# Performance work log

Hardware: AMD Instinct MI355X
Metric: run time of the kernel (lower is better)

Reference implementation:

```python
import jax, jax.numpy as jnp
import numpy as np

B, H, S, D = 2, 16, 2048, 128
BS = 128  # block_size
NB = S // BS  # num_blocks
SPARSITY_PROB = 0.5


def setup_inputs() -> dict:
    key = jax.random.key(0)
    kq, kk, kv, km = jax.random.split(key, 4)
    query = jax.random.normal(kq, (B, H, S, D), dtype=jnp.float32)
    k_ = jax.random.normal(kk, (B, H, S, D), dtype=jnp.float32)
    v_ = jax.random.normal(kv, (B, H, S, D), dtype=jnp.float32)
    # block pattern: rand < sparsity_prob, diagonal forced True (causal=False)
    block_mask = jax.random.uniform(km, (NB, NB)) < SPARSITY_PROB
    block_mask = block_mask | jnp.eye(NB, dtype=bool)
    return {"query": query, "key": k_, "value": v_,
            "block_mask": block_mask, "block_size": BS}


def reference(query, key, value, block_mask, block_size):
    b, h, s, d = query.shape
    nb = s // block_size
    scale = 1.0 / jnp.sqrt(jnp.float32(d))
    # reshape into blocks: (b, h, nb, bs, d)
    qb = query.reshape(b, h, nb, block_size, d)
    kb = key.reshape(b, h, nb, block_size, d)
    vb = value.reshape(b, h, nb, block_size, d)
    # per-(i,j)-block scores: (b, h, i, j, q, k)
    scores = jnp.einsum('bhiqd,bhjkd->bhijqk', qb, kb) * scale
    # IMPORTANT: softmax is taken independently within each block (axis=-1),
    # matching the original's per-block (non-merged) softmax.
    attn = jax.nn.softmax(scores, axis=-1)
    # zero out inactive blocks, then sum contributions over j
    attn = attn * block_mask[None, None, :, :, None, None].astype(attn.dtype)
    out = jnp.einsum('bhijqk,bhjkd->bhiqd', attn, vb)
    return out.reshape(b, h, s, d)
```

## Files before the change

kernel.cpp:

```cpp
#include <hip/hip_runtime.h>
#include <stdint.h>

#define CBDIM 256
#define WBDIM 256
#define DBDIM 512

#if __has_builtin(__builtin_amdgcn_permlane32_swap) && \
    __has_builtin(__builtin_amdgcn_permlane16_swap)
#define HAVE_PERMLANE_SWAP 1
#else
#define HAVE_PERMLANE_SWAP 0
#endif

typedef __attribute__((ext_vector_type(8))) short short8;
typedef __attribute__((ext_vector_type(4))) float f32x4;

__device__ __forceinline__ unsigned f2bf(float f) {
    union { float f; unsigned u; } a; a.f = f;
    unsigned r = a.u + 0x7fffu + ((a.u >> 16) & 1u);
    return (r >> 16) & 0xffffu;
}
__device__ __forceinline__ unsigned cvtpk_bf16(float a, float b) {
    unsigned r;
    asm("v_cvt_pk_bf16_f32 %0, %1, %2" : "=v"(r) : "v"(a), "v"(b));
    return r;
}
__device__ __forceinline__ float exp2_raw(float x) {
    float r;
    asm("v_exp_f32 %0, %1" : "=v"(r) : "v"(x));
    return r;
}
__device__ __forceinline__ float f4e(float4 v, int e) {
    return e == 0 ? v.x : e == 1 ? v.y : e == 2 ? v.z : v.w;
}
__device__ __forceinline__ unsigned u4e(uint4 v, int e) {
    return e == 0 ? v.x : e == 1 ? v.y : e == 2 ? v.z : v.w;
}
__device__ __forceinline__ uint2 shfl_u2(uint2 v, int src) {
    uint2 r;
    r.x = (unsigned)__shfl((int)v.x, src);
    r.y = (unsigned)__shfl((int)v.y, src);
    return r;
}
__device__ __forceinline__ float xor16_f(float x, int lane) {
#if HAVE_PERMLANE_SWAP
    unsigned u = __float_as_uint(x);
    auto r = __builtin_amdgcn_permlane16_swap(u, u, false, false);
    return __uint_as_float((lane & 16) ? r[0] : r[1]);
#else
    return __shfl_xor(x, 16);
#endif
}
__device__ __forceinline__ float xor32_f(float x, int lane) {
#if HAVE_PERMLANE_SWAP
    unsigned u = __float_as_uint(x);
    auto r = __builtin_amdgcn_permlane32_swap(u, u, false, false);
    return __uint_as_float((lane & 32) ? r[0] : r[1]);
#else
    return __shfl_xor(x, 32);
#endif
}
__device__ __forceinline__ bool detect_bf16(const void* p) {
    unsigned w = ((const unsigned*)p)[threadIdx.x & 63];
    unsigned lo = w & 0xffffu, ex = (lo >> 7) & 0xffu;
    bool pl = (lo == 0u) || (ex >= 0x68u && ex <= 0x86u);
    return __popcll(__ballot(pl)) >= 40;
}
__device__ __forceinline__ void gload_lds16(const void* g, void* l) {
    __builtin_amdgcn_global_load_lds(
        (const __attribute__((address_space(1))) void*)g,
        (__attribute__((address_space(3))) void*)l, 16, 0, 0);
}

__global__ __launch_bounds__(CBDIM)
void convert_fused(const void* __restrict__ Ksrc, const void* __restrict__ Vsrc,
                   uint4* __restrict__ Kw, uint4* __restrict__ Vt,
                   const unsigned char* __restrict__ Mb, int* __restrict__ order,
                   int nIdsK)
{
    const int tid = threadIdx.x;
    const int b = blockIdx.x;
    if (b < 512) {
        bool isBf = detect_bf16(Vsrc);
        if (b == 0 && tid < 64) {
            int tt = tid;
            unsigned mu = ((const unsigned*)Mb)[tt];
            bool maskByte = (__ballot((mu & 0xFFFFFF00u) != 0u) != 0ull);
            int cnt = 0;
            if (tt < 16)
                for (int j = 0; j < 16; ++j) {
                    bool a = maskByte ? (Mb[tt * 16 + j] != 0)
                                      : (((const int*)Mb)[tt * 16 + j] != 0);
                    cnt += a ? 1 : 0;
                }
            int rank = 0;
            for (int j = 0; j < 16; ++j) {
                int cj = __shfl(cnt, j);
                if (cj > cnt || (cj == cnt && j < tt)) ++rank;
            }
            if (tt < 16) order[rank] = tt;
        }
        const size_t kb = (size_t)b * 16384;
        char* base = (char*)(Vt + (size_t)b * 2048);
#pragma unroll
        for (int it = 0; it < 2; ++it) {
            int id = it * CBDIM + tid, pp = id & 31, dc = id >> 5;
            if (isBf) {
                const unsigned short* vb = (const unsigned short*)Vsrc + kb
                                           + (size_t)(4 * pp) * 128 + dc * 8;
                uint4 r0 = *(const uint4*)(vb);
                uint4 r1 = *(const uint4*)(vb + 128);
                uint4 r2 = *(const uint4*)(vb + 256);
                uint4 r3 = *(const uint4*)(vb + 384);
#pragma unroll
                for (int e = 0; e < 8; ++e) {
                    unsigned h0 = u4e(r0, e >> 1), h1 = u4e(r1, e >> 1);
                    unsigned h2 = u4e(r2, e >> 1), h3 = u4e(r3, e >> 1);
                    if (e & 1) { h0 >>= 16; h1 >>= 16; h2 >>= 16; h3 >>= 16; }
                    uint2 pk;
                    pk.x = (h0 & 0xffffu) | (h1 << 16);
                    pk.y = (h2 & 0xffffu) | (h3 << 16);
                    int d = dc * 8 + e;
                    *(uint2*)(base + d * 256 + (((pp >> 1) ^ (d & 7)) << 4)
                              + ((pp & 1) << 3)) = pk;
                }
            } else {
                const float* vb = (const float*)Vsrc + kb
                                  + (size_t)(4 * pp) * 128 + dc * 8;
                float4 ra[4], rb[4];
#pragma unroll
                for (int r = 0; r < 4; ++r) {
                    ra[r] = *(const float4*)(vb + (size_t)r * 128);
                    rb[r] = *(const float4*)(vb + (size_t)r * 128 + 4);
                }
#pragma unroll
                for (int e = 0; e < 8; ++e) {
                    float v0 = (e < 4) ? f4e(ra[0], e) : f4e(rb[0], e - 4);
                    float v1 = (e < 4) ? f4e(ra[1], e) : f4e(rb[1], e - 4);
                    float v2 = (e < 4) ? f4e(ra[2], e) : f4e(rb[2], e - 4);
                    float v3 = (e < 4) ? f4e(ra[3], e) : f4e(rb[3], e - 4);
                    uint2 pk;
                    pk.x = f2bf(v0) | (f2bf(v1) << 16);
                    pk.y = f2bf(v2) | (f2bf(v3) << 16);
                    int d = dc * 8 + e;
                    *(uint2*)(base + d * 256 + (((pp >> 1) ^ (d & 7)) << 4)
                              + ((pp & 1) << 3)) = pk;
                }
            }
        }
    } else {
        bool isBf = detect_bf16(Ksrc);
        int stride = ((int)gridDim.x - 512) * CBDIM;
        for (int id = (b - 512) * CBDIM + tid; id < nIdsK; id += stride) {
            int lid = id & 2047, tt = id >> 11;
            int r = lid >> 4, c = (lid & 15) ^ (r & 7);
            size_t eo = (size_t)tt * 16384 + (size_t)r * 128 + c * 8;
            uint4 w;
            if (isBf) {
                w = *(const uint4*)((const unsigned short*)Ksrc + eo);
            } else {
                const float* p = (const float*)Ksrc + eo;
                float4 f0 = *(const float4*)p, f1 = *(const float4*)(p + 4);
                w.x = f2bf(f0.x) | (f2bf(f0.y) << 16);
                w.y = f2bf(f0.z) | (f2bf(f0.w) << 16);
                w.z = f2bf(f1.x) | (f2bf(f1.y) << 16);
                w.w = f2bf(f1.z) | (f2bf(f1.w) << 16);
            }
            Kw[id] = w;
        }
    }
}

template<bool QF32>
__device__ __forceinline__ void attn_core(const void* Qv, const uint4* Kw,
                                          const uint4* Vt, unsigned actm,
                                          void* Ov, char* ldsK, char* ldsV,
                                          int bh, int i)
{
    constexpr int S = 2048, D = 128;
    const int tid  = threadIdx.x;
    const int lane = tid & 63;
    const int wv   = tid >> 6;
    const int quad = lane >> 4;
    const int l16  = lane & 15;

    const int qb0 = wv * 32;
    const size_t qrowbase = ((size_t)bh * S + (size_t)i * 128) * D;

    short8 qf[2][4];
#pragma unroll
    for (int nt = 0; nt < 2; ++nt) {
        int qrow = qb0 + nt * 16 + l16;
#pragma unroll
        for (int ks = 0; ks < 4; ++ks) {
            int dof = ks * 32 + quad * 8;
            if constexpr (QF32) {
                const float* qp = (const float*)Qv + qrowbase + (size_t)qrow * D + dof;
                float4 f0 = *(const float4*)qp;
                float4 f1 = *(const float4*)(qp + 4);
                short8 v;
                v[0] = (short)f2bf(f0.x); v[1] = (short)f2bf(f0.y);
                v[2] = (short)f2bf(f0.z); v[3] = (short)f2bf(f0.w);
                v[4] = (short)f2bf(f1.x); v[5] = (short)f2bf(f1.y);
                v[6] = (short)f2bf(f1.z); v[7] = (short)f2bf(f1.w);
                qf[nt][ks] = v;
            } else {
                qf[nt][ks] = *(const short8*)((const unsigned short*)Qv
                              + qrowbase + (size_t)qrow * D + dof);
            }
        }
    }

    f32x4 accO[2][8];
#pragma unroll
    for (int a = 0; a < 2; ++a)
#pragma unroll
        for (int b = 0; b < 8; ++b)
            accO[a][b] = (f32x4){0.f, 0.f, 0.f, 0.f};

    const float C2 = 0.08838834764831845f * 1.44269504088896f;

    auto STAGE = [&](const uint4* t, char* lds) {
#pragma unroll
        for (int it = 0; it < 8; ++it) {
            int id = it * WBDIM + tid;
            int lo = (it * WBDIM + wv * 64) * 16;
            gload_lds16(t + id, lds + lo);
        }
        asm volatile("" ::: "memory");
    };
    auto ktile = [&](int jj) { return Kw + (size_t)(bh * 16 + jj) * 2048; };
    auto vtile = [&](int jj) { return Vt + (size_t)(bh * 16 + jj) * 2048; };

    int j = (int)__builtin_ctz(actm);
    unsigned m = actm & (actm - 1);

    STAGE(ktile(j), ldsK);
    STAGE(vtile(j), ldsV);
    asm volatile("s_waitcnt vmcnt(8)" ::: "memory");
    asm volatile("s_barrier" ::: "memory");

    while (true) {
        int jn = m ? (int)__builtin_ctz(m) : -1;
        if (jn >= 0) m &= m - 1;

        f32x4 accS[2][8];
#pragma unroll
        for (int nt = 0; nt < 2; ++nt)
#pragma unroll
            for (int mt = 0; mt < 8; ++mt)
                accS[nt][mt] = (f32x4){0.f, 0.f, 0.f, 0.f};

#pragma unroll
        for (int mt = 0; mt < 8; ++mt) {
            int r = mt * 16 + l16;
            short8 kf[4];
#pragma unroll
            for (int ks = 0; ks < 4; ++ks) {
                int c = ks * 4 + quad;
                kf[ks] = *(const short8*)(ldsK + r * 256 + ((c ^ (r & 7)) << 4));
            }
            __builtin_amdgcn_s_setprio(1);
#pragma unroll
            for (int nt = 0; nt < 2; ++nt)
#pragma unroll
                for (int ks = 0; ks < 4; ++ks)
                    accS[nt][mt] = __builtin_amdgcn_mfma_f32_16x16x32_bf16(
                        kf[ks], qf[nt][ks], accS[nt][mt], 0, 0, 0);
            __builtin_amdgcn_s_setprio(0);
        }

        uint2 p2[2][8];
#pragma unroll
        for (int nt = 0; nt < 2; ++nt) {
            float ps[8];
#pragma unroll
            for (int mt = 0; mt < 8; ++mt) {
                f32x4 p;
#pragma unroll
                for (int rr = 0; rr < 4; ++rr)
                    p[rr] = exp2_raw(accS[nt][mt][rr] * C2);
                accS[nt][mt] = p;
                ps[mt] = (p[0] + p[1]) + (p[2] + p[3]);
            }
            float sum = ((ps[0] + ps[1]) + (ps[2] + ps[3]))
                      + ((ps[4] + ps[5]) + (ps[6] + ps[7]));
            sum += xor16_f(sum, lane);
            sum += xor32_f(sum, lane);
            float rinv = __builtin_amdgcn_rcpf(sum);
#pragma unroll
            for (int mt = 0; mt < 8; ++mt) {
                p2[nt][mt].x = cvtpk_bf16(accS[nt][mt][0] * rinv,
                                          accS[nt][mt][1] * rinv);
                p2[nt][mt].y = cvtpk_bf16(accS[nt][mt][2] * rinv,
                                          accS[nt][mt][3] * rinv);
            }
        }

        asm volatile("s_waitcnt vmcnt(0)" ::: "memory");
        asm volatile("s_barrier" ::: "memory");
        if (jn >= 0) STAGE(ktile(jn), ldsK);

#pragma unroll
        for (int ks = 0; ks < 4; ++ks) {
            short8 pf[2];
#pragma unroll
            for (int nt = 0; nt < 2; ++nt) {
#if HAVE_PERMLANE_SWAP
                unsigned ax = p2[nt][2 * ks + 0].x, ay = p2[nt][2 * ks + 0].y;
                unsigned bx = p2[nt][2 * ks + 1].x, by = p2[nt][2 * ks + 1].y;
                auto rx = __builtin_amdgcn_permlane32_swap(ax, bx, false, false);
                auto ry = __builtin_amdgcn_permlane32_swap(ay, by, false, false);
                auto sx = __builtin_amdgcn_permlane16_swap(rx[0], rx[1], false, false);
                auto sy = __builtin_amdgcn_permlane16_swap(ry[0], ry[1], false, false);
                union { uint4 u; short8 s; } w;
                w.u.x = sx[0]; w.u.y = sy[0]; w.u.z = sx[1]; w.u.w = sy[1];
                pf[nt] = w.s;
#else
                const int srcA = l16 + ((quad & 1) << 5);
                const int srcB = srcA + 16;
                const bool hiMs = (quad >> 1) != 0;
                uint2 a0 = shfl_u2(p2[nt][2 * ks + 0], srcA);
                uint2 a1 = shfl_u2(p2[nt][2 * ks + 1], srcA);
                uint2 b0 = shfl_u2(p2[nt][2 * ks + 0], srcB);
                uint2 b1 = shfl_u2(p2[nt][2 * ks + 1], srcB);
                uint2 lo, hi;
                lo.x = hiMs ? a1.x : a0.x;  lo.y = hiMs ? a1.y : a0.y;
                hi.x = hiMs ? b1.x : b0.x;  hi.y = hiMs ? b1.y : b0.y;
                union { uint4 u; short8 s; } w;
                w.u.x = lo.x; w.u.y = lo.y; w.u.z = hi.x; w.u.w = hi.y;
                pf[nt] = w.s;
#endif
            }
            __builtin_amdgcn_s_setprio(1);
#pragma unroll
            for (int dt = 0; dt < 8; ++dt) {
                int d = dt * 16 + l16;
                int c = ks * 4 + quad;
                short8 vf = *(const short8*)(ldsV + d * 256 + ((c ^ (d & 7)) << 4));
                accO[0][dt] = __builtin_amdgcn_mfma_f32_16x16x32_bf16(
                    pf[0], vf, accO[0][dt], 0, 0, 0);
                accO[1][dt] = __builtin_amdgcn_mfma_f32_16x16x32_bf16(
                    pf[1], vf, accO[1][dt], 0, 0, 0);
            }
            __builtin_amdgcn_s_setprio(0);
        }

        if (jn < 0) break;
        asm volatile("s_waitcnt vmcnt(0)" ::: "memory");
        asm volatile("s_barrier" ::: "memory");
        STAGE(vtile(jn), ldsV);
        j = jn;
    }

#pragma unroll
    for (int mt = 0; mt < 2; ++mt)
#pragma unroll
        for (int rr = 0; rr < 4; ++rr) {
            int qrow = qb0 + mt * 16 + quad * 4 + rr;
#pragma unroll
            for (int nt = 0; nt < 8; ++nt) {
                size_t idx = qrowbase + (size_t)qrow * D + nt * 16 + l16;
                if constexpr (QF32)
                    ((float*)Ov)[idx] = accO[mt][nt][rr];
                else
                    ((unsigned short*)Ov)[idx] = (unsigned short)f2bf(accO[mt][nt][rr]);
            }
        }
}

__global__ __launch_bounds__(WBDIM, 2)
void attn_ws(const void* __restrict__ Q, const uint4* __restrict__ Kw,
             const uint4* __restrict__ Vt, const unsigned char* __restrict__ Mb,
             const int* __restrict__ order, void* __restrict__ O)
{
    __shared__ uint4 ldsK4[2048];
    __shared__ uint4 ldsV4[2048];
    int blk = blockIdx.x;
    int bh = ((blk >> 7) << 3) | (blk & 7);
    int slot = (blk >> 3) & 15;
    int i = order[(blk >> 8) ? (15 - slot) : slot];
    bool qBf = detect_bf16(Q);
    unsigned mu = ((const unsigned*)Mb)[threadIdx.x & 63];
    bool maskByte = (__ballot((mu & 0xFFFFFF00u) != 0u) != 0ull);
    unsigned actm = 0;
#pragma unroll
    for (int j = 0; j < 16; ++j) {
        bool a = maskByte ? (Mb[i * 16 + j] != 0)
                          : (((const int*)Mb)[i * 16 + j] != 0);
        actm |= (a ? 1u : 0u) << j;
    }
    if (qBf)
        attn_core<false>(Q, Kw, Vt, actm, O, (char*)ldsK4, (char*)ldsV4, bh, i);
    else
        attn_core<true>(Q, Kw, Vt, actm, O, (char*)ldsK4, (char*)ldsV4, bh, i);
}

template<bool QF32, bool KVF32>
__device__ __forceinline__ void attn_body(const void* Qv, const void* Kv,
                                          const void* Vv,
                                          const unsigned char* Mb, bool maskByte,
                                          void* Ov, char* ldsK, char* ldsV,
                                          int bh, int i)
{
    constexpr int S = 2048, D = 128;
    const int tid  = threadIdx.x;
    const int lane = tid & 63;
    const int wave = tid >> 6;
    const int quad = lane >> 4;
    const int l16  = lane & 15;

    const int qb0 = wave * 16;
    const size_t qrowbase = ((size_t)bh * S + (size_t)i * 128) * D;

    short8 qf[4];
    {
        int qrow = qb0 + l16;
#pragma unroll
        for (int ks = 0; ks < 4; ++ks) {
            int dof = ks * 32 + quad * 8;
            if constexpr (QF32) {
                const float* qp = (const float*)Qv + qrowbase + (size_t)qrow * D + dof;
                float4 f0 = *(const float4*)qp;
                float4 f1 = *(const float4*)(qp + 4);
                short8 v;
                v[0] = (short)f2bf(f0.x); v[1] = (short)f2bf(f0.y);
                v[2] = (short)f2bf(f0.z); v[3] = (short)f2bf(f0.w);
                v[4] = (short)f2bf(f1.x); v[5] = (short)f2bf(f1.y);
                v[6] = (short)f2bf(f1.z); v[7] = (short)f2bf(f1.w);
                qf[ks] = v;
            } else {
                qf[ks] = *(const short8*)((const unsigned short*)Qv
                          + qrowbase + (size_t)qrow * D + dof);
            }
        }
    }

    f32x4 accO[8];
#pragma unroll
    for (int b = 0; b < 8; ++b)
        accO[b] = (f32x4){0.f, 0.f, 0.f, 0.f};

    const float C2 = 0.08838834764831845f * 1.44269504088896f;
    const int srcA = l16 + ((quad & 1) << 5);
    const int srcB = srcA + 16;
    const bool hiMs = (quad >> 1) != 0;

    for (int j = 0; j < 16; ++j) {
        bool active = maskByte ? (Mb[i * 16 + j] != 0)
                               : (((const int*)Mb)[i * 16 + j] != 0);
        if (!active) continue;

        __syncthreads();
        const size_t kb = ((size_t)bh * S + (size_t)j * 128) * D;

        if constexpr (KVF32) {
#pragma unroll
            for (int it = 0; it < 8; ++it) {
                int f = it * DBDIM + tid;
                int r = f >> 5, c4 = f & 31;
                float4 v = ((const float4*)((const float*)Kv + kb))[f];
                uint2 pk;
                pk.x = f2bf(v.x) | (f2bf(v.y) << 16);
                pk.y = f2bf(v.z) | (f2bf(v.w) << 16);
                int ch = c4 >> 1;
                *(uint2*)(ldsK + r * 256 + ((ch ^ (r & 7)) << 4)
                          + ((c4 & 1) << 3)) = pk;
            }
        } else {
#pragma unroll
            for (int it = 0; it < 4; ++it) {
                int id = it * DBDIM + tid;
                int r = id >> 4, ch = id & 15;
                uint4 v = ((const uint4*)((const unsigned short*)Kv + kb))[id];
                *(uint4*)(ldsK + r * 256 + ((ch ^ (r & 7)) << 4)) = v;
            }
        }

        {
            int id = tid, pp = id & 31, dc = id >> 5;
            if constexpr (KVF32) {
                const float* vb = (const float*)Vv + kb + (size_t)(4 * pp) * D + dc * 8;
                float4 ra[4], rb[4];
#pragma unroll
                for (int r = 0; r < 4; ++r) {
                    ra[r] = *(const float4*)(vb + (size_t)r * D);
                    rb[r] = *(const float4*)(vb + (size_t)r * D + 4);
                }
#pragma unroll
                for (int e = 0; e < 8; ++e) {
                    float v0 = (e < 4) ? f4e(ra[0], e) : f4e(rb[0], e - 4);
                    float v1 = (e < 4) ? f4e(ra[1], e) : f4e(rb[1], e - 4);
                    float v2 = (e < 4) ? f4e(ra[2], e) : f4e(rb[2], e - 4);
                    float v3 = (e < 4) ? f4e(ra[3], e) : f4e(rb[3], e - 4);
                    uint2 pk;
                    pk.x = f2bf(v0) | (f2bf(v1) << 16);
                    pk.y = f2bf(v2) | (f2bf(v3) << 16);
                    int d = dc * 8 + e;
                    *(uint2*)(ldsV + d * 256 + (((pp >> 1) ^ (d & 7)) << 4)
                              + ((pp & 1) << 3)) = pk;
                }
            } else {
                const unsigned short* vb = (const unsigned short*)Vv + kb
                                           + (size_t)(4 * pp) * D + dc * 8;
                uint4 r0 = *(const uint4*)(vb);
                uint4 r1 = *(const uint4*)(vb + D);
                uint4 r2 = *(const uint4*)(vb + 2 * D);
                uint4 r3 = *(const uint4*)(vb + 3 * D);
#pragma unroll
                for (int e = 0; e < 8; ++e) {
                    unsigned h0 = u4e(r0, e >> 1), h1 = u4e(r1, e >> 1);
                    unsigned h2 = u4e(r2, e >> 1), h3 = u4e(r3, e >> 1);
                    if (e & 1) { h0 >>= 16; h1 >>= 16; h2 >>= 16; h3 >>= 16; }
                    uint2 pk;
                    pk.x = (h0 & 0xffffu) | (h1 << 16);
                    pk.y = (h2 & 0xffffu) | (h3 << 16);
                    int d = dc * 8 + e;
                    *(uint2*)(ldsV + d * 256 + (((pp >> 1) ^ (d & 7)) << 4)
                              + ((pp & 1) << 3)) = pk;
                }
            }
        }
        __syncthreads();

        f32x4 accS[8];
#pragma unroll
        for (int mt = 0; mt < 8; ++mt)
            accS[mt] = (f32x4){0.f, 0.f, 0.f, 0.f};

#pragma unroll
        for (int mt = 0; mt < 8; ++mt) {
            int r = mt * 16 + l16;
            short8 kf[4];
#pragma unroll
            for (int ks = 0; ks < 4; ++ks) {
                int c = ks * 4 + quad;
                kf[ks] = *(const short8*)(ldsK + r * 256 + ((c ^ (r & 7)) << 4));
            }
#pragma unroll
            for (int ks = 0; ks < 4; ++ks)
                accS[mt] = __builtin_amdgcn_mfma_f32_16x16x32_bf16(
                    kf[ks], qf[ks], accS[mt], 0, 0, 0);
        }

        float ps[8];
#pragma unroll
        for (int mt = 0; mt < 8; ++mt) {
            f32x4 p;
#pragma unroll
            for (int rr = 0; rr < 4; ++rr)
                p[rr] = exp2f(accS[mt][rr] * C2);
            accS[mt] = p;
            ps[mt] = (p[0] + p[1]) + (p[2] + p[3]);
        }
        float sum = ((ps[0] + ps[1]) + (ps[2] + ps[3]))
                  + ((ps[4] + ps[5]) + (ps[6] + ps[7]));
        sum += __shfl_xor(sum, 16);
        sum += __shfl_xor(sum, 32);
        float rinv = 1.0f / sum;

        uint2 p2[8];
#pragma unroll
        for (int mt = 0; mt < 8; ++mt) {
            p2[mt].x = f2bf(accS[mt][0] * rinv) | (f2bf(accS[mt][1] * rinv) << 16);
            p2[mt].y = f2bf(accS[mt][2] * rinv) | (f2bf(accS[mt][3] * rinv) << 16);
        }

#pragma unroll
        for (int ks = 0; ks < 4; ++ks) {
            short8 pf;
            {
                uint2 a0 = shfl_u2(p2[2 * ks + 0], srcA);
                uint2 a1 = shfl_u2(p2[2 * ks + 1], srcA);
                uint2 b0 = shfl_u2(p2[2 * ks + 0], srcB);
                uint2 b1 = shfl_u2(p2[2 * ks + 1], srcB);
                uint2 lo, hi;
                lo.x = hiMs ? a1.x : a0.x;  lo.y = hiMs ? a1.y : a0.y;
                hi.x = hiMs ? b1.x : b0.x;  hi.y = hiMs ? b1.y : b0.y;
                union { uint4 u; short8 s; } w;
                w.u.x = lo.x; w.u.y = lo.y; w.u.z = hi.x; w.u.w = hi.y;
                pf = w.s;
            }
#pragma unroll
            for (int dt = 0; dt < 8; ++dt) {
                int d = dt * 16 + l16;
                int c = ks * 4 + quad;
                short8 vf = *(const short8*)(ldsV + d * 256 + ((c ^ (d & 7)) << 4));
                accO[dt] = __builtin_amdgcn_mfma_f32_16x16x32_bf16(
                    pf, vf, accO[dt], 0, 0, 0);
            }
        }
    }

#pragma unroll
    for (int rr = 0; rr < 4; ++rr) {
        int qrow = qb0 + quad * 4 + rr;
#pragma unroll
        for (int dt = 0; dt < 8; ++dt) {
            size_t idx = qrowbase + (size_t)qrow * D + dt * 16 + l16;
            if constexpr (QF32)
                ((float*)Ov)[idx] = accO[dt][rr];
            else
                ((unsigned short*)Ov)[idx] = (unsigned short)f2bf(accO[dt][rr]);
        }
    }
}

__global__ __launch_bounds__(DBDIM, 4)
void attn_direct(const void* __restrict__ Q, const void* __restrict__ K,
                 const void* __restrict__ V,
                 const unsigned char* __restrict__ Mb, void* __restrict__ O)
{
    __shared__ uint4 ldsK4[2048];
    __shared__ uint4 ldsV4[2048];
    int blk = blockIdx.x;
    int bh = ((blk >> 7) << 3) | (blk & 7);
    int i  = (blk >> 3) & 15;
    bool qBf = detect_bf16(Q);
    unsigned mu = ((const unsigned*)Mb)[threadIdx.x & 63];
    bool maskByte = (__ballot((mu & 0xFFFFFF00u) != 0u) != 0ull);
    if (qBf)
        attn_body<false, false>(Q, K, V, Mb, maskByte, O,
                                (char*)ldsK4, (char*)ldsV4, bh, i);
    else
        attn_body<true, true>(Q, K, V, Mb, maskByte, O,
                              (char*)ldsK4, (char*)ldsV4, bh, i);
}

extern "C" void kernel_launch(void* const* d_in, const int* in_sizes, int n_in,
                              void* d_out, int out_size, void* d_ws, size_t ws_size,
                              hipStream_t stream) {
    const int NIDS = 512 * 2048;
    const size_t need = (size_t)NIDS * 16 * 2 + 256;
    if (ws_size >= need) {
        uint4* Kw = (uint4*)d_ws;
        uint4* Vt = Kw + NIDS;
        int* order = (int*)(Vt + NIDS);
        convert_fused<<<1536, CBDIM, 0, stream>>>(d_in[1], d_in[2], Kw, Vt,
                                                  (const unsigned char*)d_in[3],
                                                  order, NIDS);
        attn_ws<<<512, WBDIM, 0, stream>>>(d_in[0], Kw, Vt,
                                           (const unsigned char*)d_in[3],
                                           order, d_out);
    } else {
        attn_direct<<<512, DBDIM, 0, stream>>>(d_in[0], d_in[1], d_in[2],
                                               (const unsigned char*)d_in[3], d_out);
    }
}
```

Measured before the change: 187.7 us.

## Load V fragments directly from global in MFMA layout; double-buffer K in LDS

The prep kernel now writes V pre-arranged in per-lane MFMA fragment order, so the attention kernel can load V operands straight into registers with global_load_dwordx4 instead of staging through LDS. The freed LDS becomes a second K buffer, so the next K tile is prefetched while the current block is computed. V fragment loads are software-pipelined across ks steps using two register sets. This removes the V LDS round trip and one barrier per block, at the cost of more VGPRs and reliance on the L2 cache for V reads.

```diff
diff --git a/kernel.cpp b/kernel.cpp
--- a/kernel.cpp
+++ b/kernel.cpp
@@ -102,6 +102,13 @@
         }
         const size_t kb = (size_t)b * 16384;
         char* base = (char*)(Vt + (size_t)b * 2048);
+        auto vaddr = [&](int pp, int d) -> size_t {
+            int c = pp >> 1;
+            int ks = c >> 2, qd = c & 3;
+            int dt = d >> 4, s16 = d & 15;
+            return (size_t)((((ks * 8 + dt) * 64 + qd * 16 + s16) << 4)
+                            + ((pp & 1) << 3));
+        };
 #pragma unroll
         for (int it = 0; it < 2; ++it) {
             int id = it * CBDIM + tid, pp = id & 31, dc = id >> 5;
@@ -120,9 +127,7 @@
                     uint2 pk;
                     pk.x = (h0 & 0xffffu) | (h1 << 16);
                     pk.y = (h2 & 0xffffu) | (h3 << 16);
-                    int d = dc * 8 + e;
-                    *(uint2*)(base + d * 256 + (((pp >> 1) ^ (d & 7)) << 4)
-                              + ((pp & 1) << 3)) = pk;
+                    *(uint2*)(base + vaddr(pp, dc * 8 + e)) = pk;
                 }
             } else {
                 const float* vb = (const float*)Vsrc + kb
@@ -142,9 +147,7 @@
                     uint2 pk;
                     pk.x = f2bf(v0) | (f2bf(v1) << 16);
                     pk.y = f2bf(v2) | (f2bf(v3) << 16);
-                    int d = dc * 8 + e;
-                    *(uint2*)(base + d * 256 + (((pp >> 1) ^ (d & 7)) << 4)
-                              + ((pp & 1) << 3)) = pk;
+                    *(uint2*)(base + vaddr(pp, dc * 8 + e)) = pk;
                 }
             }
         }
@@ -174,8 +177,7 @@
 template<bool QF32>
 __device__ __forceinline__ void attn_core(const void* Qv, const uint4* Kw,
                                           const uint4* Vt, unsigned actm,
-                                          void* Ov, char* ldsK, char* ldsV,
-                                          int bh, int i)
+                                          void* Ov, char* ldsK, int bh, int i)
 {
     constexpr int S = 2048, D = 128;
     const int tid  = threadIdx.x;
@@ -230,20 +232,33 @@
         asm volatile("" ::: "memory");
     };
     auto ktile = [&](int jj) { return Kw + (size_t)(bh * 16 + jj) * 2048; };
-    auto vtile = [&](int jj) { return Vt + (size_t)(bh * 16 + jj) * 2048; };
+    auto vtile = [&](int jj) {
+        return (const char*)(Vt + (size_t)(bh * 16 + jj) * 2048);
+    };
 
     int j = (int)__builtin_ctz(actm);
     unsigned m = actm & (actm - 1);
 
     STAGE(ktile(j), ldsK);
-    STAGE(vtile(j), ldsV);
-    asm volatile("s_waitcnt vmcnt(8)" ::: "memory");
+    asm volatile("s_waitcnt vmcnt(0)" ::: "memory");
     asm volatile("s_barrier" ::: "memory");
+    int cur = 0;
+
+    uint4 vfA[8], vfB[8];
 
     while (true) {
         int jn = m ? (int)__builtin_ctz(m) : -1;
         if (jn >= 0) m &= m - 1;
 
+        char* kbuf = ldsK + (cur << 15);
+        if (jn >= 0) STAGE(ktile(jn), ldsK + ((cur ^ 1) << 15));
+
+        const char* vlane = vtile(j) + (size_t)lane * 16;
+#pragma unroll
+        for (int dt = 0; dt < 8; ++dt)
+            asm volatile("global_load_dwordx4 %0, %1, off"
+                         : "=v"(vfA[dt]) : "v"(vlane + dt * 1024));
+
         f32x4 accS[2][8];
 #pragma unroll
         for (int nt = 0; nt < 2; ++nt)
@@ -258,7 +273,7 @@
 #pragma unroll
             for (int ks = 0; ks < 4; ++ks) {
                 int c = ks * 4 + quad;
-                kf[ks] = *(const short8*)(ldsK + r * 256 + ((c ^ (r & 7)) << 4));
+                kf[ks] = *(const short8*)(kbuf + r * 256 + ((c ^ (r & 7)) << 4));
             }
             __builtin_amdgcn_s_setprio(1);
 #pragma unroll
@@ -296,10 +311,6 @@
                                           accS[nt][mt][3] * rinv);
             }
         }
-
-        asm volatile("s_waitcnt vmcnt(0)" ::: "memory");
-        asm volatile("s_barrier" ::: "memory");
-        if (jn >= 0) STAGE(ktile(jn), ldsK);
 
 #pragma unroll
         for (int ks = 0; ks < 4; ++ks) {
@@ -332,24 +343,37 @@
                 pf[nt] = w.s;
 #endif
             }
+            if (ks < 3) {
+                const char* vb2 = vlane + (ks + 1) * 8192;
+#pragma unroll
+                for (int dt = 0; dt < 8; ++dt) {
+                    if (ks & 1)
+                        asm volatile("global_load_dwordx4 %0, %1, off"
+                                     : "=v"(vfA[dt]) : "v"(vb2 + dt * 1024));
+                    else
+                        asm volatile("global_load_dwordx4 %0, %1, off"
+                                     : "=v"(vfB[dt]) : "v"(vb2 + dt * 1024));
+                }
+            }
+            if (ks < 3) asm volatile("s_waitcnt vmcnt(8)" ::: "memory");
+            else        asm volatile("s_waitcnt vmcnt(0)" ::: "memory");
+            __builtin_amdgcn_sched_barrier(0);
             __builtin_amdgcn_s_setprio(1);
 #pragma unroll
             for (int dt = 0; dt < 8; ++dt) {
-                int d = dt * 16 + l16;
-                int c = ks * 4 + quad;
-                short8 vf = *(const short8*)(ldsV + d * 256 + ((c ^ (d & 7)) << 4));
+                union { uint4 u; short8 s; } w;
+                w.u = (ks & 1) ? vfB[dt] : vfA[dt];
                 accO[0][dt] = __builtin_amdgcn_mfma_f32_16x16x32_bf16(
-                    pf[0], vf, accO[0][dt], 0, 0, 0);
+                    pf[0], w.s, accO[0][dt], 0, 0, 0);
                 accO[1][dt] = __builtin_amdgcn_mfma_f32_16x16x32_bf16(
-                    pf[1], vf, accO[1][dt], 0, 0, 0);
+                    pf[1], w.s, accO[1][dt], 0, 0, 0);
             }
             __builtin_amdgcn_s_setprio(0);
         }
 
         if (jn < 0) break;
-        asm volatile("s_waitcnt vmcnt(0)" ::: "memory");
         asm volatile("s_barrier" ::: "memory");
-        STAGE(vtile(jn), ldsV);
+        cur ^= 1;
         j = jn;
     }
 
@@ -374,8 +398,7 @@
              const uint4* __restrict__ Vt, const unsigned char* __restrict__ Mb,
              const int* __restrict__ order, void* __restrict__ O)
 {
-    __shared__ uint4 ldsK4[2048];
-    __shared__ uint4 ldsV4[2048];
+    __shared__ uint4 ldsK4[4096];
     int blk = blockIdx.x;
     int bh = ((blk >> 7) << 3) | (blk & 7);
     int slot = (blk >> 3) & 15;
@@ -391,9 +414,9 @@
         actm |= (a ? 1u : 0u) << j;
     }
     if (qBf)
-        attn_core<false>(Q, Kw, Vt, actm, O, (char*)ldsK4, (char*)ldsV4, bh, i);
+        attn_core<false>(Q, Kw, Vt, actm, O, (char*)ldsK4, bh, i);
     else
-        attn_core<true>(Q, Kw, Vt, actm, O, (char*)ldsK4, (char*)ldsV4, bh, i);
+        attn_core<true>(Q, Kw, Vt, actm, O, (char*)ldsK4, bh, i);
 }
 
 template<bool QF32, bool KVF32>
```

Result: no change. 189.0 us (median of 2 runs) (+0.7%).
